# Performance work log

Measured on AMD Instinct MI355X. Metric: run time of the kernel, lower is better.

The kernel has to match this reference:

```python
import jax, jax.numpy as jnp
import numpy as np

INFEAT = 4096
OUTFEAT = 11008
TOKENS = 2048


def setup_inputs() -> dict:
    key = jax.random.key(0)
    k1, k2, k3, k4, k5 = jax.random.split(key, 5)
    x = jax.random.normal(k1, (TOKENS, INFEAT), dtype=jnp.float32)
    # Random uint8 int-weights, packed 4-per-uint32 exactly like pack():
    # word = w1 | w2<<8 | w3<<16 | w4<<24, rows grouped along infeatures.
    wbytes = jax.random.randint(k2, (INFEAT // 4, 4, OUTFEAT), 0, 256, dtype=jnp.int32).astype(jnp.uint32)
    qweight = (wbytes[:, 0] | (wbytes[:, 1] << 8) | (wbytes[:, 2] << 16) | (wbytes[:, 3] << 24))
    qweight = qweight.astype(jnp.int32)  # same bit pattern as uint32 buffer
    scales = (jax.random.uniform(k3, (OUTFEAT,), dtype=jnp.float32) * 0.01 + 1e-4)
    zeros = jax.random.randint(k4, (OUTFEAT,), 0, 256, dtype=jnp.int32)  # uint8 zero points
    bias = jax.random.normal(k5, (OUTFEAT,), dtype=jnp.float32) * 0.01
    return {"x": x, "qweight": qweight, "scales": scales, "zeros": zeros, "bias": bias}


def _dequant(qweight, scales, zeros):
    q = qweight.astype(jnp.uint32)  # [INFEAT//4, OUTFEAT]
    b0 = (q & 0xFF)
    b1 = ((q >> 8) & 0xFF)
    b2 = ((q >> 16) & 0xFF)
    b3 = ((q >> 24) & 0xFF)
    w_int = jnp.stack([b0, b1, b2, b3], axis=1).reshape(-1, q.shape[-1])  # [INFEAT, OUTFEAT]
    # pack(): int = round(w/scale) + zero  =>  w = (int - zero) * scale (per output channel)
    return (w_int.astype(jnp.float32) - zeros.astype(jnp.float32)[None, :]) * scales[None, :]


def reference(x, qweight, scales, zeros, bias):
    w = _dequant(qweight, scales, zeros)          # [INFEAT, OUTFEAT]
    return x @ w + bias[None, :]                  # [TOKENS, OUTFEAT]
```

## Files before the change

### kernel.cpp

```cpp
#include <hip/hip_runtime.h>
#include <hip/hip_bf16.h>

#define INFEAT 4096
#define OUTFEAT 11008
#define TOKENS 2048

typedef int v4i __attribute__((ext_vector_type(4)));
typedef __bf16 bf16_t;
typedef bf16_t bf16x4 __attribute__((ext_vector_type(4)));
typedef bf16_t bf16x8 __attribute__((ext_vector_type(8)));
typedef float f32x4 __attribute__((ext_vector_type(4)));

__device__ __forceinline__ void async_copy16(const void* g, void* l) {
    __builtin_amdgcn_global_load_lds((const __attribute__((address_space(1))) void*)g,
                                     (__attribute__((address_space(3))) void*)l,
                                     16, 0, 0);
}

__global__ __launch_bounds__(256) void quant_x(
    const float* __restrict__ x, unsigned int* __restrict__ xq,
    float* __restrict__ xscale, int* __restrict__ xsum)
{
    __shared__ float smax[4];
    __shared__ int ssum[4];
    const int row = blockIdx.x;
    const int tid = threadIdx.x;
    const int lane = tid & 63, wid = tid >> 6;
    const float* xr = x + (size_t)row * INFEAT;

    float4 v[4];
    #pragma unroll
    for (int i = 0; i < 4; ++i) v[i] = *(const float4*)&xr[tid * 16 + i * 4];

    float am = 0.f;
    #pragma unroll
    for (int i = 0; i < 4; ++i)
        am = fmaxf(am, fmaxf(fmaxf(fabsf(v[i].x), fabsf(v[i].y)),
                             fmaxf(fabsf(v[i].z), fabsf(v[i].w))));
    #pragma unroll
    for (int o = 32; o > 0; o >>= 1) am = fmaxf(am, __shfl_xor(am, o, 64));
    if (lane == 0) smax[wid] = am;
    __syncthreads();
    am = fmaxf(fmaxf(smax[0], smax[1]), fmaxf(smax[2], smax[3]));
    const float inv = am > 0.f ? 127.0f / am : 0.f;
    const float sc  = am > 0.f ? am / 127.0f : 0.f;

    int lsum = 0;
    unsigned int pk[4];
    #pragma unroll
    for (int i = 0; i < 4; ++i) {
        int q0 = (int)rintf(fminf(fmaxf(v[i].x * inv, -127.f), 127.f));
        int q1 = (int)rintf(fminf(fmaxf(v[i].y * inv, -127.f), 127.f));
        int q2 = (int)rintf(fminf(fmaxf(v[i].z * inv, -127.f), 127.f));
        int q3 = (int)rintf(fminf(fmaxf(v[i].w * inv, -127.f), 127.f));
        lsum += q0 + q1 + q2 + q3;
        pk[i] = (q0 & 255) | ((q1 & 255) << 8) | ((q2 & 255) << 16) | ((unsigned)(q3 & 255) << 24);
    }
    *(uint4*)&xq[(size_t)row * (INFEAT / 4) + tid * 4] = *(uint4*)pk;

    #pragma unroll
    for (int o = 32; o > 0; o >>= 1) lsum += __shfl_xor(lsum, o, 64);
    if (lane == 0) ssum[wid] = lsum;
    __syncthreads();
    if (tid == 0) {
        xsum[row] = ssum[0] + ssum[1] + ssum[2] + ssum[3];
        xscale[row] = sc;
    }
}

__global__ __launch_bounds__(256) void t_w(
    const unsigned int* __restrict__ qw, unsigned char* __restrict__ wt)
{
    __shared__ unsigned int Tw[64 * 64];
    const int n0 = blockIdx.x * 64;
    const int kp0 = blockIdx.y * 64;
    const int tn = threadIdx.x & 63;
    const int tk4 = threadIdx.x >> 6;

    #pragma unroll
    for (int it = 0; it < 16; ++it) {
        const int kp = tk4 * 16 + it;
        const unsigned int q = qw[(size_t)(kp0 + kp) * OUTFEAT + n0 + tn] ^ 0x80808080u;
        const int slot = (kp >> 2) ^ (tn & 15);
        Tw[tn * 64 + slot * 4 + (kp & 3)] = q;
    }
    __syncthreads();

    #pragma unroll
    for (int i = 0; i < 4; ++i) {
        const int flat = i * 256 + threadIdx.x;
        const int n = flat >> 4;
        const int c = flat & 15;
        uint4 v = *(const uint4*)&Tw[n * 64 + ((c ^ (n & 15)) * 4)];
        *(uint4*)&wt[(size_t)(n0 + n) * INFEAT + (size_t)kp0 * 4 + c * 16] = v;
    }
}

__global__ __launch_bounds__(256, 2) void q3gemm_i8d(
    const unsigned char* __restrict__ xqb, const unsigned char* __restrict__ wt,
    const float* __restrict__ scales, const int* __restrict__ zeros,
    const float* __restrict__ bias, const float* __restrict__ xscale,
    const int* __restrict__ xsum, float* __restrict__ out)
{
    __shared__ unsigned char Als[2][128 * 128];
    __shared__ unsigned char Bls[2][128 * 128];

    const int tid = threadIdx.x;
    const int n0 = (blockIdx.x >> 4) * 128;
    const int m0 = (blockIdx.x & 15) * 128;

    const int wid = tid >> 6, lane = tid & 63;
    const int wm = (wid & 1) * 64, wn = (wid >> 1) * 64;
    const int lr = lane & 15, lq = lane >> 4;

    const int rb0  = wid * 32;
    const int rsub = lane >> 3;
    const int sl   = lane & 7;

    v4i acc[4][4];
    #pragma unroll
    for (int i = 0; i < 4; ++i)
        #pragma unroll
        for (int j = 0; j < 4; ++j)
            acc[i][j] = (v4i){0, 0, 0, 0};

#define STAGE(T, C) do {                                                              \
    const int kk0_ = (T) * 128;                                                       \
    _Pragma("unroll")                                                                 \
    for (int p_ = 0; p_ < 4; ++p_) {                                                  \
        const int r_ = rb0 + p_ * 8 + rsub;                                           \
        const int s_ = sl ^ (r_ & 7);                                                 \
        async_copy16(&xqb[(size_t)(m0 + r_) * INFEAT + kk0_ + s_ * 16],               \
                     &Als[C][(rb0 + p_ * 8) * 128]);                                  \
    }                                                                                 \
    _Pragma("unroll")                                                                 \
    for (int p_ = 0; p_ < 4; ++p_) {                                                  \
        const int r_ = rb0 + p_ * 8 + rsub;                                           \
        const int s_ = sl ^ (r_ & 7);                                                 \
        async_copy16(&wt[(size_t)(n0 + r_) * INFEAT + kk0_ + s_ * 16],                \
                     &Bls[C][(rb0 + p_ * 8) * 128]);                                  \
    }                                                                                 \
} while (0)

    const int NT = INFEAT / 128;

    STAGE(0, 0);
    STAGE(1, 1);
    asm volatile("s_waitcnt vmcnt(8)" ::: "memory");
    __builtin_amdgcn_sched_barrier(0);
    __builtin_amdgcn_s_barrier();
    __builtin_amdgcn_sched_barrier(0);

    for (int t = 0; t < NT; ++t) {
        const int cur = t & 1;
        const unsigned char* Ab = Als[cur];
        const unsigned char* Bb = Bls[cur];

        v4i af[2][4], bfv[2][4];
        #pragma unroll
        for (int ks = 0; ks < 2; ++ks)
            #pragma unroll
            for (int q = 0; q < 4; ++q) {
                const int ra = wm + q * 16 + lr;
                const int pa = (ks * 4 + lq) ^ (ra & 7);
                af[ks][q] = *(const v4i*)&Ab[ra * 128 + pa * 16];
                const int rb = wn + q * 16 + lr;
                const int pb = (ks * 4 + lq) ^ (rb & 7);
                bfv[ks][q] = *(const v4i*)&Bb[rb * 128 + pb * 16];
            }
        asm volatile("s_waitcnt lgkmcnt(0)" ::: "memory");
        __builtin_amdgcn_sched_barrier(0);
        __builtin_amdgcn_s_barrier();
        __builtin_amdgcn_sched_barrier(0);

        if (t + 2 < NT) STAGE(t + 2, cur);

        #pragma unroll
        for (int ks = 0; ks < 2; ++ks)
            #pragma unroll
            for (int i = 0; i < 4; ++i)
                #pragma unroll
                for (int j = 0; j < 4; ++j)
                    acc[i][j] = __builtin_amdgcn_mfma_i32_16x16x64_i8(af[ks][i], bfv[ks][j], acc[i][j], 0, 0, 0);

        __builtin_amdgcn_sched_barrier(0);
        if (t < NT - 2) { asm volatile("s_waitcnt vmcnt(8)" ::: "memory"); }
        else            { asm volatile("s_waitcnt vmcnt(0)" ::: "memory"); }
        __builtin_amdgcn_sched_barrier(0);
        __builtin_amdgcn_s_barrier();
        __builtin_amdgcn_sched_barrier(0);
    }
#undef STAGE

    #pragma unroll
    for (int j = 0; j < 4; ++j) {
        const int col = n0 + wn + j * 16 + lr;
        const float sn = scales[col];
        const int zi = 128 - zeros[col];
        const float bv = bias[col];
        #pragma unroll
        for (int i = 0; i < 4; ++i) {
            const int rb = m0 + wm + i * 16 + lq * 4;
            #pragma unroll
            for (int r = 0; r < 4; ++r) {
                const int tot = acc[i][j][r] + zi * xsum[rb + r];
                out[(size_t)(rb + r) * OUTFEAT + col] = xscale[rb + r] * sn * (float)tot + bv;
            }
        }
    }
}

#define LDSS 72
__global__ __launch_bounds__(256) void q3gemm_fb(
    const float* __restrict__ x, const unsigned int* __restrict__ qw,
    const float* __restrict__ scales, const int* __restrict__ zeros,
    const float* __restrict__ bias, float* __restrict__ out)
{
    __shared__ bf16_t Als[128 * LDSS];
    __shared__ bf16_t Bls[128 * LDSS];
    const int tid = threadIdx.x;
    const int m0 = blockIdx.y * 128;
    const int n0 = blockIdx.x * 128;
    const int bcol = tid & 127;
    const int bpr  = tid >> 7;
    const float scf = scales[n0 + bcol];
    const float nzs = (float)zeros[n0 + bcol] * scf;
    const int acolg = tid & 15;
    const int arow0 = tid >> 4;
    const int wid  = tid >> 6;
    const int lane = tid & 63;
    const int wm = (wid & 1) * 64;
    const int wn = (wid >> 1) * 64;
    const int lr = lane & 15;
    const int lq = lane >> 4;
    f32x4 acc[4][4];
    #pragma unroll
    for (int i = 0; i < 4; ++i)
        #pragma unroll
        for (int j = 0; j < 4; ++j) acc[i][j] = (f32x4)0.0f;
    for (int kt = 0; kt < INFEAT / 64; ++kt) {
        const int k0 = kt * 64;
        #pragma unroll
        for (int p = 0; p < 8; ++p) {
            const int row = arow0 + p * 16;
            const float4 v = *(const float4*)&x[(size_t)(m0 + row) * INFEAT + k0 + acolg * 4];
            bf16x4 b;
            b[0] = (bf16_t)v.x; b[1] = (bf16_t)v.y; b[2] = (bf16_t)v.z; b[3] = (bf16_t)v.w;
            *(bf16x4*)&Als[row * LDSS + acolg * 4] = b;
        }
        const int kp0 = k0 >> 2;
        #pragma unroll
        for (int it = 0; it < 8; ++it) {
            const int prel = it * 2 + bpr;
            const unsigned int q = qw[(size_t)(kp0 + prel) * OUTFEAT + n0 + bcol];
            bf16x4 b;
            b[0] = (bf16_t)((float)(q & 0xFFu)        * scf - nzs);
            b[1] = (bf16_t)((float)((q >> 8) & 0xFFu) * scf - nzs);
            b[2] = (bf16_t)((float)((q >> 16) & 0xFFu)* scf - nzs);
            b[3] = (bf16_t)((float)(q >> 24)          * scf - nzs);
            *(bf16x4*)&Bls[bcol * LDSS + prel * 4] = b;
        }
        __syncthreads();
        #pragma unroll
        for (int ks = 0; ks < 2; ++ks) {
            bf16x8 af[4], bfv[4];
            #pragma unroll
            for (int t = 0; t < 4; ++t) {
                af[t]  = *(const bf16x8*)&Als[(wm + t * 16 + lr) * LDSS + ks * 32 + lq * 8];
                bfv[t] = *(const bf16x8*)&Bls[(wn + t * 16 + lr) * LDSS + ks * 32 + lq * 8];
            }
            #pragma unroll
            for (int i = 0; i < 4; ++i)
                #pragma unroll
                for (int j = 0; j < 4; ++j)
                    acc[i][j] = __builtin_amdgcn_mfma_f32_16x16x32_bf16(af[i], bfv[j], acc[i][j], 0, 0, 0);
        }
        __syncthreads();
    }
    #pragma unroll
    for (int j = 0; j < 4; ++j) {
        const int col = n0 + wn + j * 16 + lr;
        const float bv = bias[col];
        #pragma unroll
        for (int i = 0; i < 4; ++i) {
            const int rbs = m0 + wm + i * 16 + lq * 4;
            #pragma unroll
            for (int r = 0; r < 4; ++r)
                out[(size_t)(rbs + r) * OUTFEAT + col] = acc[i][j][r] + bv;
        }
    }
}

extern "C" void kernel_launch(void* const* d_in, const int* in_sizes, int n_in,
                              void* d_out, int out_size, void* d_ws, size_t ws_size,
                              hipStream_t stream) {
    const float*        x      = (const float*)d_in[0];
    const unsigned int* qw     = (const unsigned int*)d_in[1];
    const float*        scales = (const float*)d_in[2];
    const int*          zeros  = (const int*)d_in[3];
    const float*        bias   = (const float*)d_in[4];
    float*              out    = (float*)d_out;

    const size_t wt_bytes = (size_t)OUTFEAT * INFEAT;
    const size_t xq_bytes = (size_t)TOKENS * INFEAT;
    const size_t need = wt_bytes + xq_bytes + TOKENS * (sizeof(float) + sizeof(int)) + 256;

    if (ws_size >= need) {
        unsigned char* wt = (unsigned char*)d_ws;
        unsigned int* xq  = (unsigned int*)((char*)d_ws + wt_bytes);
        float* xscale = (float*)((char*)d_ws + wt_bytes + xq_bytes);
        int*   xsum   = (int*)((char*)d_ws + wt_bytes + xq_bytes + TOKENS * sizeof(float));

        quant_x<<<dim3(TOKENS), dim3(256), 0, stream>>>(x, xq, xscale, xsum);
        t_w<<<dim3(OUTFEAT / 64, (INFEAT / 4) / 64), dim3(256), 0, stream>>>(qw, wt);
        q3gemm_i8d<<<dim3((OUTFEAT / 128) * (TOKENS / 128)), dim3(256), 0, stream>>>(
            (const unsigned char*)xq, wt, scales, zeros, bias, xscale, xsum, out);
    } else {
        q3gemm_fb<<<dim3(OUTFEAT / 128, TOKENS / 128), dim3(256), 0, stream>>>(
            x, qw, scales, zeros, bias, out);
    }
}
```

Before: 267.1 us.

## Merge activation quantization and weight transpose into one prep kernel, remap GEMM blocks

```diff
diff --git a/kernel.cpp b/kernel.cpp
--- a/kernel.cpp
+++ b/kernel.cpp
@@ -17,82 +17,86 @@
                                      16, 0, 0);
 }
 
-__global__ __launch_bounds__(256) void quant_x(
-    const float* __restrict__ x, unsigned int* __restrict__ xq,
-    float* __restrict__ xscale, int* __restrict__ xsum)
+__global__ __launch_bounds__(256) void prep(
+    const float* __restrict__ x, const unsigned int* __restrict__ qw,
+    unsigned int* __restrict__ xq, float* __restrict__ xscale, int* __restrict__ xsum,
+    unsigned char* __restrict__ wt)
 {
+    __shared__ unsigned int Tw[64 * 64];
     __shared__ float smax[4];
     __shared__ int ssum[4];
-    const int row = blockIdx.x;
     const int tid = threadIdx.x;
-    const int lane = tid & 63, wid = tid >> 6;
-    const float* xr = x + (size_t)row * INFEAT;
-
-    float4 v[4];
-    #pragma unroll
-    for (int i = 0; i < 4; ++i) v[i] = *(const float4*)&xr[tid * 16 + i * 4];
-
-    float am = 0.f;
-    #pragma unroll
-    for (int i = 0; i < 4; ++i)
-        am = fmaxf(am, fmaxf(fmaxf(fabsf(v[i].x), fabsf(v[i].y)),
-                             fmaxf(fabsf(v[i].z), fabsf(v[i].w))));
-    #pragma unroll
-    for (int o = 32; o > 0; o >>= 1) am = fmaxf(am, __shfl_xor(am, o, 64));
-    if (lane == 0) smax[wid] = am;
-    __syncthreads();
-    am = fmaxf(fmaxf(smax[0], smax[1]), fmaxf(smax[2], smax[3]));
-    const float inv = am > 0.f ? 127.0f / am : 0.f;
-    const float sc  = am > 0.f ? am / 127.0f : 0.f;
-
-    int lsum = 0;
-    unsigned int pk[4];
-    #pragma unroll
-    for (int i = 0; i < 4; ++i) {
-        int q0 = (int)rintf(fminf(fmaxf(v[i].x * inv, -127.f), 127.f));
-        int q1 = (int)rintf(fminf(fmaxf(v[i].y * inv, -127.f), 127.f));
-        int q2 = (int)rintf(fminf(fmaxf(v[i].z * inv, -127.f), 127.f));
-        int q3 = (int)rintf(fminf(fmaxf(v[i].w * inv, -127.f), 127.f));
-        lsum += q0 + q1 + q2 + q3;
-        pk[i] = (q0 & 255) | ((q1 & 255) << 8) | ((q2 & 255) << 16) | ((unsigned)(q3 & 255) << 24);
-    }
-    *(uint4*)&xq[(size_t)row * (INFEAT / 4) + tid * 4] = *(uint4*)pk;
-
-    #pragma unroll
-    for (int o = 32; o > 0; o >>= 1) lsum += __shfl_xor(lsum, o, 64);
-    if (lane == 0) ssum[wid] = lsum;
-    __syncthreads();
-    if (tid == 0) {
-        xsum[row] = ssum[0] + ssum[1] + ssum[2] + ssum[3];
-        xscale[row] = sc;
-    }
-}
-
-__global__ __launch_bounds__(256) void t_w(
-    const unsigned int* __restrict__ qw, unsigned char* __restrict__ wt)
-{
-    __shared__ unsigned int Tw[64 * 64];
-    const int n0 = blockIdx.x * 64;
-    const int kp0 = blockIdx.y * 64;
-    const int tn = threadIdx.x & 63;
-    const int tk4 = threadIdx.x >> 6;
-
-    #pragma unroll
-    for (int it = 0; it < 16; ++it) {
-        const int kp = tk4 * 16 + it;
-        const unsigned int q = qw[(size_t)(kp0 + kp) * OUTFEAT + n0 + tn] ^ 0x80808080u;
-        const int slot = (kp >> 2) ^ (tn & 15);
-        Tw[tn * 64 + slot * 4 + (kp & 3)] = q;
-    }
-    __syncthreads();
-
-    #pragma unroll
-    for (int i = 0; i < 4; ++i) {
-        const int flat = i * 256 + threadIdx.x;
-        const int n = flat >> 4;
-        const int c = flat & 15;
-        uint4 v = *(const uint4*)&Tw[n * 64 + ((c ^ (n & 15)) * 4)];
-        *(uint4*)&wt[(size_t)(n0 + n) * INFEAT + (size_t)kp0 * 4 + c * 16] = v;
+
+    if (blockIdx.x < 2752) {
+        const int bid = blockIdx.x;
+        const int n0  = (bid % 172) * 64;
+        const int kp0 = (bid / 172) * 64;
+        const int tn4 = tid & 15;
+        const int kb  = tid >> 4;
+        #pragma unroll
+        for (int it = 0; it < 4; ++it) {
+            const int kp = kb + it * 16;
+            uint4 q = *(const uint4*)&qw[(size_t)(kp0 + kp) * OUTFEAT + n0 + tn4 * 4];
+            q.x ^= 0x80808080u; q.y ^= 0x80808080u; q.z ^= 0x80808080u; q.w ^= 0x80808080u;
+            const int ks = kp >> 2, kq = kp & 3;
+            const int n = tn4 * 4;
+            Tw[(n + 0) * 64 + ((ks ^ ((n + 0) & 15)) << 2) + kq] = q.x;
+            Tw[(n + 1) * 64 + ((ks ^ ((n + 1) & 15)) << 2) + kq] = q.y;
+            Tw[(n + 2) * 64 + ((ks ^ ((n + 2) & 15)) << 2) + kq] = q.z;
+            Tw[(n + 3) * 64 + ((ks ^ ((n + 3) & 15)) << 2) + kq] = q.w;
+        }
+        __syncthreads();
+        #pragma unroll
+        for (int i = 0; i < 4; ++i) {
+            const int flat = i * 256 + tid;
+            const int n = flat >> 4;
+            const int c = flat & 15;
+            uint4 v = *(const uint4*)&Tw[n * 64 + ((c ^ (n & 15)) * 4)];
+            *(uint4*)&wt[(size_t)(n0 + n) * INFEAT + (size_t)kp0 * 4 + c * 16] = v;
+        }
+    } else {
+        const int row = blockIdx.x - 2752;
+        const int lane = tid & 63, wid = tid >> 6;
+        const float* xr = x + (size_t)row * INFEAT;
+
+        float4 v[4];
+        #pragma unroll
+        for (int i = 0; i < 4; ++i) v[i] = *(const float4*)&xr[tid * 16 + i * 4];
+
+        float am = 0.f;
+        #pragma unroll
+        for (int i = 0; i < 4; ++i)
+            am = fmaxf(am, fmaxf(fmaxf(fabsf(v[i].x), fabsf(v[i].y)),
+                                 fmaxf(fabsf(v[i].z), fabsf(v[i].w))));
+        #pragma unroll
+        for (int o = 32; o > 0; o >>= 1) am = fmaxf(am, __shfl_xor(am, o, 64));
+        if (lane == 0) smax[wid] = am;
+        __syncthreads();
+        am = fmaxf(fmaxf(smax[0], smax[1]), fmaxf(smax[2], smax[3]));
+        const float inv = am > 0.f ? 127.0f / am : 0.f;
+        const float sc  = am > 0.f ? am / 127.0f : 0.f;
+
+        int lsum = 0;
+        unsigned int pk[4];
+        #pragma unroll
+        for (int i = 0; i < 4; ++i) {
+            int q0 = (int)rintf(fminf(fmaxf(v[i].x * inv, -127.f), 127.f));
+            int q1 = (int)rintf(fminf(fmaxf(v[i].y * inv, -127.f), 127.f));
+            int q2 = (int)rintf(fminf(fmaxf(v[i].z * inv, -127.f), 127.f));
+            int q3 = (int)rintf(fminf(fmaxf(v[i].w * inv, -127.f), 127.f));
+            lsum += q0 + q1 + q2 + q3;
+            pk[i] = (q0 & 255) | ((q1 & 255) << 8) | ((q2 & 255) << 16) | ((unsigned)(q3 & 255) << 24);
+        }
+        *(uint4*)&xq[(size_t)row * (INFEAT / 4) + tid * 4] = *(uint4*)pk;
+
+        #pragma unroll
+        for (int o = 32; o > 0; o >>= 1) lsum += __shfl_xor(lsum, o, 64);
+        if (lane == 0) ssum[wid] = lsum;
+        __syncthreads();
+        if (tid == 0) {
+            xsum[row] = ssum[0] + ssum[1] + ssum[2] + ssum[3];
+            xscale[row] = sc;
+        }
     }
 }
 
@@ -106,8 +110,9 @@
     __shared__ unsigned char Bls[2][128 * 128];
 
     const int tid = threadIdx.x;
-    const int n0 = (blockIdx.x >> 4) * 128;
-    const int m0 = (blockIdx.x & 15) * 128;
+    const int sbid = (blockIdx.x & 7) * 172 + (blockIdx.x >> 3);
+    const int n0 = (sbid >> 4) * 128;
+    const int m0 = (sbid & 15) * 128;
 
     const int wid = tid >> 6, lane = tid & 63;
     const int wm = (wid & 1) * 64, wn = (wid >> 1) * 64;
@@ -311,8 +316,7 @@
         float* xscale = (float*)((char*)d_ws + wt_bytes + xq_bytes);
         int*   xsum   = (int*)((char*)d_ws + wt_bytes + xq_bytes + TOKENS * sizeof(float));
 
-        quant_x<<<dim3(TOKENS), dim3(256), 0, stream>>>(x, xq, xscale, xsum);
-        t_w<<<dim3(OUTFEAT / 64, (INFEAT / 4) / 64), dim3(256), 0, stream>>>(qw, wt);
+        prep<<<dim3(2752 + TOKENS), dim3(256), 0, stream>>>(x, qw, xq, xscale, xsum, wt);
         q3gemm_i8d<<<dim3((OUTFEAT / 128) * (TOKENS / 128)), dim3(256), 0, stream>>>(
             (const unsigned char*)xq, wt, scales, zeros, bias, xscale, xsum, out);
     } else {
```

After: 266.7 us. Within noise of the previous version (-0.1%).
